# Kernel tuning notes

Hardware: AMD Instinct MI355X
Metric: run time of the kernel (lower is better)

The kernel has to match this reference:

```python
import jax, jax.numpy as jnp
import numpy as np

NUM_HEADS = 8
LN_EPS = 1e-5
COS_EPS = 1e-8


def setup_inputs() -> dict:
    key = jax.random.key(0)
    ks = jax.random.split(key, 16)
    B, S, H, C = 16, 4096, 768, 64
    std = 0.02
    f32 = jnp.float32
    return {
        "hidden_states": jax.random.normal(ks[0], (B, S, H), f32),
        "concept_embeddings": jax.random.normal(ks[1], (C, H), f32),
        "Wq": jax.random.normal(ks[2], (H, H), f32) * std,
        "bq": jnp.zeros((H,), f32),
        "Wk": jax.random.normal(ks[3], (H, H), f32) * std,
        "bk": jnp.zeros((H,), f32),
        "Wv": jax.random.normal(ks[4], (H, H), f32) * std,
        "bv": jnp.zeros((H,), f32),
        "Wo": jax.random.normal(ks[5], (H, H), f32) * std,
        "bo": jnp.zeros((H,), f32),
        "Wg1": jax.random.normal(ks[6], (3 * H, H), f32) * std,
        "bg1": jnp.zeros((H,), f32),
        "Wg2": jax.random.normal(ks[7], (H, 1), f32) * std,
        "bg2": jnp.zeros((1,), f32),
        "ln_g": jnp.ones((H,), f32),
        "ln_b": jnp.zeros((H,), f32),
    }


def reference(hidden_states, concept_embeddings, Wq, bq, Wk, bk, Wv, bv,
              Wo, bo, Wg1, bg1, Wg2, bg2, ln_g, ln_b):
    B, S, H = hidden_states.shape
    C = concept_embeddings.shape[0]
    NH = NUM_HEADS
    HD = H // NH

    # QKV projections; concepts are shared across the batch
    Q = (hidden_states @ Wq + bq).reshape(B, S, NH, HD)      # [B,S,NH,HD]
    K = (concept_embeddings @ Wk + bk).reshape(C, NH, HD)    # [C,NH,HD]
    V = (concept_embeddings @ Wv + bv).reshape(C, NH, HD)

    scores = jnp.einsum('bshd,chd->bhsc', Q, K) / (HD ** 0.5)  # [B,NH,S,C]
    attn = jax.nn.softmax(scores, axis=-1)  # dropout is eval-mode identity
    context = jnp.einsum('bhsc,chd->bshd', attn, V).reshape(B, S, H)
    context = context @ Wo + bo

    # content relevance: cosine sim of mean-pooled text vs mean-pooled concepts
    text_pooled = hidden_states.mean(axis=1)          # [B,H]
    concept_pooled = concept_embeddings.mean(axis=0)  # [H] (same for all batch)
    num = text_pooled @ concept_pooled                # [B]
    den = jnp.maximum(jnp.linalg.norm(text_pooled, axis=-1), COS_EPS) * \
          jnp.maximum(jnp.linalg.norm(concept_pooled), COS_EPS)
    relevance = num / den                             # [B]
    rel_feat = jnp.broadcast_to(relevance[:, None, None], (B, S, H))

    gate_in = jnp.concatenate([hidden_states, context, rel_feat], axis=-1)  # [B,S,3H]
    gate = jax.nn.sigmoid(jax.nn.relu(gate_in @ Wg1 + bg1) @ Wg2 + bg2)     # [B,S,1]

    out = hidden_states + gate * context
    mu = out.mean(axis=-1, keepdims=True)
    var = out.var(axis=-1, keepdims=True)
    out = (out - mu) / jnp.sqrt(var + LN_EPS) * ln_g + ln_b

    attn_avg = attn.mean(axis=1)  # [B,S,C] for XAI
    return out, attn_avg
```

## Files before the change

### kernel.cpp

```cpp
#include <hip/hip_runtime.h>

typedef __attribute__((ext_vector_type(8))) short bf16x8;
typedef __attribute__((ext_vector_type(4))) float f32x4;
typedef unsigned short u16;

#define MFMA(a,b,c) __builtin_amdgcn_mfma_f32_16x16x32_bf16((a),(b),(c),0,0,0)

__device__ __forceinline__ short f2bf(float f){
  union { float f; unsigned u; } v; v.f = f;
  unsigned r = v.u + 0x7FFFu + ((v.u >> 16) & 1u);
  return (short)(r >> 16);
}
__device__ __forceinline__ float bf2f(short s){
  union { unsigned u; float f; } v; v.u = ((unsigned)(unsigned short)s) << 16; return v.f;
}
__device__ __forceinline__ bf16x8 pack8(f32x4 x, f32x4 y){
  bf16x8 r;
  r[0]=f2bf(x[0]); r[1]=f2bf(x[1]); r[2]=f2bf(x[2]); r[3]=f2bf(x[3]);
  r[4]=f2bf(y[0]); r[5]=f2bf(y[1]); r[6]=f2bf(y[2]); r[7]=f2bf(y[3]);
  return r;
}
__device__ __forceinline__ int pch(int c, int row){ return (c & ~7) | ((c & 7) ^ (row & 7)); }

__device__ __forceinline__ void gload16(void* lp, const void* gp){
  __builtin_amdgcn_global_load_lds((const __attribute__((address_space(1))) unsigned*)gp,
                                   (__attribute__((address_space(3))) unsigned*)lp, 16, 0, 0);
}
__device__ __forceinline__ void stWB(short* buf, const short* img, int half, int w, int lane){
  const char* gp = (const char*)img;
  #pragma unroll
  for (int it=0; it<4; ++it){
    int id = it*256 + w*64 + lane; int r = id>>3, c = id&7;
    gload16((char*)buf + it*4096 + w*1024, gp + r*256 + half*128 + c*16);
  }
}
__device__ __forceinline__ void stA128(short* buf, const u16* rowb, int kstep, int w, int lane){
  #pragma unroll
  for (int it=0; it<4; ++it){
    int id = it*256 + w*64 + lane; int r = id>>3, c = id&7;
    gload16((char*)buf + it*4096 + w*1024, rowb + (size_t)r*1536 + (kstep*8 + c)*8);
  }
}
__device__ __forceinline__ void stA256(short* buf, const u16* rowb, int kstep, int w, int lane){
  int tid = w*64 + lane;
  #pragma unroll
  for (int it=0; it<4; ++it){
    int id = it*512 + tid; int r = id>>3, c = id&7;
    gload16((char*)buf + it*8192 + w*1024, rowb + (size_t)r*1536 + (kstep*8 + c)*8);
  }
}
__device__ __forceinline__ void stB256(short* buf, const short* img, int half, int w, int lane){
  int tid = w*64 + lane;
  #pragma unroll
  for (int it=0; it<4; ++it){
    int id = it*512 + tid; int r = id>>3, c = id&7;
    gload16((char*)buf + it*8192 + w*1024,
            img + (size_t)(r>>7)*98304 + (size_t)(r&127)*128 + half*64 + c*8);
  }
}

__global__ void prep_w(const float* __restrict__ Wg1, short* __restrict__ WaI, short* __restrict__ WbI){
  __shared__ short lt[128][136];
  int blk = blockIdx.x;
  int mat = blk / 36, t = blk % 36, kt = t / 6, jt = t % 6;
  const float* src = (mat==0)? Wg1 : (Wg1 + (size_t)768*768);
  short* dst = (mat==0)? WaI : WbI;
  int tid = threadIdx.x;
  #pragma unroll
  for (int it=0; it<16; ++it){
    int kl = it*8 + (tid>>5);
    int jl = (tid&31)*4;
    f32x4 v = *(const f32x4*)&src[(size_t)(kt*128+kl)*768 + jt*128 + jl];
    lt[jl+0][kl]=f2bf(v[0]); lt[jl+1][kl]=f2bf(v[1]);
    lt[jl+2][kl]=f2bf(v[2]); lt[jl+3][kl]=f2bf(v[3]);
  }
  __syncthreads();
  size_t base = (size_t)(jt*6 + kt)*16384;
  #pragma unroll
  for (int cc=0; cc<8; ++cc){
    int ci = cc*256 + tid;
    int jl = ci >> 4, sc = ci & 15;
    int kkb = ((sc ^ (jl & 7)) << 3);
    bf16x8 v = *(const bf16x8*)&lt[jl][kkb];
    *(bf16x8*)&dst[base + (size_t)jl*128 + sc*8] = v;
  }
}

__global__ __launch_bounds__(256) void prep_kv(const float* __restrict__ ce,
                        const float* __restrict__ Wk, const float* __restrict__ bk,
                        const float* __restrict__ Wv, const float* __restrict__ bv,
                        short* __restrict__ Kc, short* __restrict__ VT){
  __shared__ float sh[8][768];
  int jt = blockIdx.x / 8, cg = blockIdx.x % 8;
  int tid = threadIdx.x;
  int j = jt*64 + (tid & 63);
  int cl = tid >> 6;
  for (int i = tid; i < 8*768; i += 256){
    int c2 = i / 768; int h = i - c2*768;
    sh[c2][h] = ce[(size_t)(cg*8+c2)*768 + h];
  }
  __syncthreads();
  float aK0=0.f, aV0=0.f, aK1=0.f, aV1=0.f;
  #pragma unroll 4
  for (int h=0; h<768; ++h){
    float wk = Wk[(size_t)h*768 + j];
    float wv = Wv[(size_t)h*768 + j];
    float x0 = sh[cl*2][h], x1 = sh[cl*2+1][h];
    aK0 += x0*wk; aV0 += x0*wv;
    aK1 += x1*wk; aV1 += x1*wv;
  }
  float bkj = bk[j], bvj = bv[j];
  int c0 = cg*8 + cl*2;
  Kc[(size_t)c0*768 + j]     = f2bf(aK0 + bkj);
  Kc[(size_t)(c0+1)*768 + j] = f2bf(aK1 + bkj);
  VT[(size_t)j*64 + c0]      = f2bf(aV0 + bvj);
  VT[(size_t)j*64 + c0+1]    = f2bf(aV1 + bvj);
}

__global__ void prep_misc(const float* __restrict__ Wg1, const float* __restrict__ ce,
                          const float* __restrict__ bq, const short* __restrict__ Kc,
                          float* __restrict__ wg1c, float* __restrict__ cp,
                          float* __restrict__ sbias){
  __shared__ float red[4][64];
  int b = blockIdx.x, tid = threadIdx.x;
  if (b < 12){
    int j = b*64 + (tid & 63);
    int kq = tid >> 6;
    float s = 0.f;
    for (int r=0; r<192; ++r)
      s += Wg1[(size_t)(1536 + kq*192 + r)*768 + j];
    red[kq][tid&63] = s;
    __syncthreads();
    if (tid < 64) wg1c[b*64+tid] = red[0][tid]+red[1][tid]+red[2][tid]+red[3][tid];
  } else if (b < 15){
    int h = (b-12)*256 + tid;
    float s = 0.f;
    #pragma unroll
    for (int c2=0; c2<64; ++c2) s += ce[(size_t)c2*768 + h];
    cp[h] = s * (1.f/64.f);
  } else {
    int hc = (b-15)*256 + tid;
    int h = hc >> 6, c = hc & 63;
    float s = 0.f;
    #pragma unroll
    for (int j=0; j<96; ++j)
      s += bq[h*96+j] * bf2f(Kc[(size_t)c*768 + h*96 + j]);
    sbias[hc] = s * 0.10206207262f;
  }
}

__global__ __launch_bounds__(256) void prep_eff(const float* __restrict__ Wq,
                        const short* __restrict__ Kc, short* __restrict__ WeffI){
  __shared__ short KA[64][104];
  __shared__ short WB[128][104];
  int h = blockIdx.x / 6, kt = blockIdx.x % 6, tid = threadIdx.x;
  const int lane = tid & 63, w = tid >> 6, l15 = lane & 15, g = lane >> 4;
  #pragma unroll
  for (int it=0; it<3; ++it){
    int i = it*256 + tid;
    int c = i / 12, cb = i % 12;
    *(bf16x8*)&KA[c][cb*8] = *(const bf16x8*)&Kc[(size_t)c*768 + h*96 + cb*8];
  }
  #pragma unroll
  for (int it=0; it<12; ++it){
    int i = it*256 + tid;
    int d = i / 24, q = i % 24;
    f32x4 v = *(const f32x4*)&Wq[(size_t)(kt*128+d)*768 + h*96 + q*4];
    WB[d][q*4+0]=f2bf(v[0]); WB[d][q*4+1]=f2bf(v[1]);
    WB[d][q*4+2]=f2bf(v[2]); WB[d][q*4+3]=f2bf(v[3]);
  }
  __syncthreads();
  f32x4 acc[4][2];
  #pragma unroll
  for (int i=0;i<4;++i){ acc[i][0]=(f32x4){0,0,0,0}; acc[i][1]=(f32x4){0,0,0,0}; }
  #pragma unroll
  for (int ks=0; ks<3; ++ks){
    bf16x8 a[4], b[2];
    #pragma unroll
    for (int mf=0; mf<4; ++mf) a[mf] = *(const bf16x8*)&KA[mf*16+l15][ks*32+g*8];
    #pragma unroll
    for (int nf=0; nf<2; ++nf) b[nf] = *(const bf16x8*)&WB[w*32+nf*16+l15][ks*32+g*8];
    #pragma unroll
    for (int mf=0; mf<4; ++mf)
      #pragma unroll
      for (int nf=0; nf<2; ++nf)
        acc[mf][nf] = MFMA(a[mf], b[nf], acc[mf][nf]);
  }
  size_t base = (size_t)((h>>1)*6 + kt)*16384;
  #pragma unroll
  for (int mf=0; mf<4; ++mf)
    #pragma unroll
    for (int nf=0; nf<2; ++nf)
      #pragma unroll
      for (int r=0; r<4; ++r){
        int c = mf*16 + g*4 + r;
        int d = w*32 + nf*16 + l15;
        int hcl = (h&1)*64 + c;
        WeffI[base + (size_t)hcl*128 + (((d>>3)^(hcl&7))<<3) + (d&7)] = f2bf(acc[mf][nf][r] * 0.10206207262f);
      }
}

__global__ __launch_bounds__(256) void prep_vwo(const float* __restrict__ Wo,
                        const short* __restrict__ VT, short* __restrict__ VWoI){
  __shared__ short WoT[128][104];
  __shared__ short VA[64][104];
  int h = blockIdx.x / 6, dt = blockIdx.x % 6, tid = threadIdx.x;
  const int lane = tid & 63, w = tid >> 6, l15 = lane & 15, g = lane >> 4;
  #pragma unroll
  for (int it=0; it<12; ++it){
    int i = it*256 + tid;
    int j = i / 32, qd = i % 32;
    f32x4 v = *(const f32x4*)&Wo[(size_t)(h*96+j)*768 + dt*128 + qd*4];
    WoT[qd*4+0][j]=f2bf(v[0]); WoT[qd*4+1][j]=f2bf(v[1]);
    WoT[qd*4+2][j]=f2bf(v[2]); WoT[qd*4+3][j]=f2bf(v[3]);
  }
  #pragma unroll
  for (int it=0; it<3; ++it){
    int i = it*256 + tid;
    int j = i / 8, cb = i % 8;
    bf16x8 v = *(const bf16x8*)&VT[(size_t)(h*96+j)*64 + cb*8];
    #pragma unroll
    for (int x=0; x<8; ++x) VA[cb*8+x][j] = v[x];
  }
  __syncthreads();
  f32x4 acc[2][4];
  #pragma unroll
  for (int i=0;i<2;++i)
    #pragma unroll
    for (int j=0;j<4;++j) acc[i][j]=(f32x4){0,0,0,0};
  #pragma unroll
  for (int ks=0; ks<3; ++ks){
    bf16x8 a[2], b[4];
    #pragma unroll
    for (int mf=0; mf<2; ++mf) a[mf] = *(const bf16x8*)&WoT[w*32+mf*16+l15][ks*32+g*8];
    #pragma unroll
    for (int nf=0; nf<4; ++nf) b[nf] = *(const bf16x8*)&VA[nf*16+l15][ks*32+g*8];
    #pragma unroll
    for (int mf=0; mf<2; ++mf)
      #pragma unroll
      for (int nf=0; nf<4; ++nf)
        acc[mf][nf] = MFMA(a[mf], b[nf], acc[mf][nf]);
  }
  size_t base = (size_t)(dt*4 + (h>>1))*16384;
  #pragma unroll
  for (int mf=0; mf<2; ++mf)
    #pragma unroll
    for (int nf=0; nf<4; ++nf)
      #pragma unroll
      for (int r=0; r<4; ++r){
        int d = w*32 + mf*16 + g*4 + r;
        int c = nf*16 + l15;
        int hcl = (h&1)*64 + c;
        VWoI[base + (size_t)d*128 + (((hcl>>3)^(d&7))<<3) + (hcl&7)] = f2bf(acc[mf][nf][r]);
      }
}

__global__ __launch_bounds__(384) void prep_hs(const float* __restrict__ hs,
                                               float* __restrict__ outp, float* __restrict__ tpp){
  __shared__ float csum[4][768];
  int tid = threadIdx.x;
  int c = tid % 96, rg = tid / 96;
  size_t r0 = (size_t)blockIdx.x * 128;
  u16* holes = (u16*)outp;
  float s[8];
  #pragma unroll
  for (int j=0;j<8;++j) s[j]=0.f;
  #pragma unroll 4
  for (int i=0; i<32; ++i){
    size_t row = r0 + rg*32 + i;
    const float* p = hs + row*768 + c*8;
    f32x4 x = __builtin_nontemporal_load((const f32x4*)p);
    f32x4 y = __builtin_nontemporal_load((const f32x4*)(p+4));
    *(bf16x8*)&holes[row*1536 + pch(c,(int)row)*8] = pack8(x,y);
    #pragma unroll
    for (int j=0;j<4;++j){ s[j]+=x[j]; s[4+j]+=y[j]; }
  }
  #pragma unroll
  for (int j=0;j<8;++j) csum[rg][c*8+j] = s[j];
  __syncthreads();
  for (int cc=tid; cc<768; cc+=384)
    tpp[(size_t)blockIdx.x*768 + cc] = csum[0][cc]+csum[1][cc]+csum[2][cc]+csum[3][cc];
}

__global__ void pool23(const float* __restrict__ tpp, const float* __restrict__ cp,
                       float* __restrict__ rel){
  int b = blockIdx.x;
  float a=0.f, n1=0.f, n2=0.f;
  for (int h = threadIdx.x; h < 768; h += 256){
    float s = 0.f;
    #pragma unroll
    for (int k=0; k<32; ++k) s += tpp[((size_t)b*32 + k)*768 + h];
    s *= (1.f/4096.f);
    float c = cp[h];
    a += s*c; n1 += s*s; n2 += c*c;
  }
  #pragma unroll
  for (int m=1; m<64; m<<=1){ a+=__shfl_xor(a,m); n1+=__shfl_xor(n1,m); n2+=__shfl_xor(n2,m); }
  __shared__ float r3[3][4];
  int w = threadIdx.x >> 6;
  if ((threadIdx.x & 63) == 0){ r3[0][w]=a; r3[1][w]=n1; r3[2][w]=n2; }
  __syncthreads();
  if (threadIdx.x == 0){
    float A = r3[0][0]+r3[0][1]+r3[0][2]+r3[0][3];
    float N1= r3[1][0]+r3[1][1]+r3[1][2]+r3[1][3];
    float N2= r3[2][0]+r3[2][1]+r3[2][2]+r3[2][3];
    rel[b] = A / (fmaxf(sqrtf(N1),1e-8f) * fmaxf(sqrtf(N2),1e-8f));
  }
}

__global__ __launch_bounds__(256) void gs(const short* __restrict__ WeffI,
                                          const float* __restrict__ sbias, float* outp){
  __shared__ short A0[8192], A1[8192], B0[8192], B1[8192];
  const int tid = threadIdx.x, lane = tid & 63, w = tid >> 6;
  const int l15 = lane & 15, g = lane >> 4;
  const int bid = blockIdx.x;
  const int nb = (bid >> 3) & 3, mt = (bid/32)*8 + (bid & 7);
  const int wm = w & 1, wn = w >> 1;
  const size_t t0 = (size_t)mt*128;
  u16* holes = (u16*)outp;
  const u16* Arow = holes + t0*1536;
  const short* Wimg = WeffI + (size_t)nb*6*16384;
  f32x4 acc[4][4];
  #pragma unroll
  for (int i=0;i<4;++i)
    #pragma unroll
    for (int j=0;j<4;++j) acc[i][j] = (f32x4){0.f,0.f,0.f,0.f};
  stA128(A0, Arow, 0, w, lane);
  stWB(B0, Wimg, 0, w, lane);
  __syncthreads();
  #pragma unroll
  for (int ks2=0; ks2<12; ++ks2){
    const short* Ac = (ks2&1)? A1 : A0;
    const short* Bc = (ks2&1)? B1 : B0;
    short* An = (ks2&1)? A0 : A1;
    short* Bn = (ks2&1)? B0 : B1;
    if (ks2<11){
      stA128(An, Arow, ks2+1, w, lane);
      stWB(Bn, Wimg + (size_t)(((ks2+1)>>1))*16384, (ks2+1)&1, w, lane);
    }
    #pragma unroll
    for (int ks=0; ks<2; ++ks){
      bf16x8 a[4], b[4];
      #pragma unroll
      for (int mf=0; mf<4; ++mf){ int r = wm*64+mf*16+l15; a[mf] = *(const bf16x8*)&Ac[r*64 + (((ks*4+g)^(r&7))<<3)]; }
      #pragma unroll
      for (int nf=0; nf<4; ++nf){ int r = wn*64+nf*16+l15; b[nf] = *(const bf16x8*)&Bc[r*64 + (((ks*4+g)^(r&7))<<3)]; }
      #pragma unroll
      for (int mf=0; mf<4; ++mf)
        #pragma unroll
        for (int nf=0; nf<4; ++nf)
          acc[mf][nf] = MFMA(a[mf], b[nf], acc[mf][nf]);
    }
    __syncthreads();
  }
  #pragma unroll
  for (int mf=0; mf<4; ++mf)
    #pragma unroll
    for (int r=0; r<4; ++r){
      float v[4];
      #pragma unroll
      for (int nf=0; nf<4; ++nf)
        v[nf] = acc[mf][nf][r] + sbias[nb*128 + wn*64 + nf*16 + l15];
      float m = fmaxf(fmaxf(v[0],v[1]), fmaxf(v[2],v[3]));
      m = fmaxf(m,__shfl_xor(m,1)); m = fmaxf(m,__shfl_xor(m,2));
      m = fmaxf(m,__shfl_xor(m,4)); m = fmaxf(m,__shfl_xor(m,8));
      float e[4]; float s = 0.f;
      #pragma unroll
      for (int nf=0; nf<4; ++nf){ e[nf] = __expf(v[nf]-m); s += e[nf]; }
      s += __shfl_xor(s,1); s += __shfl_xor(s,2); s += __shfl_xor(s,4); s += __shfl_xor(s,8);
      float inv = 1.f/s;
      int grow = wm*64 + mf*16 + g*4 + r;
      #pragma unroll
      for (int nf=0; nf<4; ++nf){
        int col = nb*128 + wn*64 + nf*16 + l15;
        holes[(t0+grow)*1536 + 768 + pch(col>>3, grow)*8 + (col&7)] = (u16)f2bf(e[nf]*inv);
      }
    }
}

__global__ __launch_bounds__(256) void gvwo(const short* __restrict__ VWoI,
                                            const float* __restrict__ bo, float* outp){
  __shared__ short B0[8192], B1[8192];
  const int tid = threadIdx.x, lane = tid & 63, w = tid >> 6;
  const int l15 = lane & 15, g = lane >> 4;
  const size_t t0 = (size_t)blockIdx.x * 64;
  const int arow = w*16 + l15;
  const int drow = w*16 + g*4;
  u16* holes = (u16*)outp;
  bf16x8 af[16];
  #pragma unroll
  for (int kk=0; kk<16; ++kk){
    int kc = kk*4 + g;
    af[kk] = *(const bf16x8*)&holes[(t0+arow)*1536 + 768 + pch(kc, arow)*8];
  }
  stWB(B0, VWoI, 0, w, lane);
  {
    float s0[8], s1[8];
    #pragma unroll
    for (int j=0;j<8;++j){ s0[j]=0.f; s1[j]=0.f; }
    #pragma unroll
    for (int kk=0; kk<16; kk+=2)
      #pragma unroll
      for (int j=0;j<8;++j) s0[j] += bf2f(af[kk][j]);
    #pragma unroll
    for (int kk=1; kk<16; kk+=2)
      #pragma unroll
      for (int j=0;j<8;++j) s1[j] += bf2f(af[kk][j]);
    float* ap = &outp[(size_t)50331648 + (size_t)(t0+arow)*64];
    f32x4 o;
    #pragma unroll
    for (int j=0;j<4;++j) o[j] = s0[j]*0.125f;
    __builtin_nontemporal_store(o, (f32x4*)(ap + g*8));
    #pragma unroll
    for (int j=0;j<4;++j) o[j] = s0[4+j]*0.125f;
    __builtin_nontemporal_store(o, (f32x4*)(ap + g*8 + 4));
    #pragma unroll
    for (int j=0;j<4;++j) o[j] = s1[j]*0.125f;
    __builtin_nontemporal_store(o, (f32x4*)(ap + (4+g)*8));
    #pragma unroll
    for (int j=0;j<4;++j) o[j] = s1[4+j]*0.125f;
    __builtin_nontemporal_store(o, (f32x4*)(ap + (4+g)*8 + 4));
  }
  __syncthreads();
  #pragma unroll 1
  for (int nb=0; nb<6; ++nb){
    f32x4 acc[8];
    #pragma unroll
    for (int i=0;i<8;++i) acc[i]=(f32x4){0.f,0.f,0.f,0.f};
    #pragma unroll
    for (int ks2=0; ks2<8; ++ks2){
      const short* Bc = (ks2&1)? B1 : B0;
      short* Bn = (ks2&1)? B0 : B1;
      if (ks2<7)       stWB(Bn, VWoI + (size_t)(nb*4 + ((ks2+1)>>1))*16384, (ks2+1)&1, w, lane);
      else if (nb<5)   stWB(Bn, VWoI + (size_t)((nb+1)*4)*16384, 0, w, lane);
      #pragma unroll
      for (int ks=0; ks<2; ++ks){
        bf16x8 a = af[ks2*2 + ks];
        #pragma unroll
        for (int nf=0; nf<8; ++nf){
          int br = nf*16 + l15;
          bf16x8 b = *(const bf16x8*)&Bc[br*64 + (((ks*4+g)^(br&7))<<3)];
          acc[nf] = MFMA(a, b, acc[nf]);
        }
      }
      __syncthreads();
    }
    #pragma unroll
    for (int nf=0; nf<8; ++nf)
      #pragma unroll
      for (int r=0; r<4; ++r){
        int row = drow + r;
        int col = nb*128 + nf*16 + l15;
        float v = acc[nf][r] + bo[col];
        holes[(t0+row)*1536 + 768 + pch(col>>3, row)*8 + (col&7)] = (u16)f2bf(v);
      }
  }
}

__global__ void __launch_bounds__(512)
__attribute__((amdgpu_waves_per_eu(2, 2))) gate_mm(const short* __restrict__ WaI,
    const short* __restrict__ WbI, const float* __restrict__ bg1,
    const float* __restrict__ wg1c, const float* __restrict__ Wg2,
    const float* __restrict__ rel, float* __restrict__ gpart, float* outp){
  extern __shared__ char lds[];
  short* A0 = (short*)lds;
  short* A1 = (short*)(lds + 32768);
  short* B0 = (short*)(lds + 65536);
  short* B1 = (short*)(lds + 98304);
  const int tid = threadIdx.x, lane = tid & 63, w = tid >> 6;
  const int l15 = lane & 15, g = lane >> 4;
  const int bid = blockIdx.x;
  const int nb = (bid >> 3) % 3, mt = (bid/24)*8 + (bid & 7);
  const int wm = w & 1, wn = w >> 1;
  const size_t t0 = (size_t)mt*256;
  const float relb = rel[t0 >> 12];
  u16* holes = (u16*)outp;
  const u16* h1p = holes + t0*1536;
  const u16* h2p = h1p + 768;
  f32x4 acc[8][4];
  #pragma unroll
  for (int i=0;i<8;++i)
    #pragma unroll
    for (int j=0;j<4;++j) acc[i][j]=(f32x4){0.f,0.f,0.f,0.f};
  stA256(A0, h1p, 0, w, lane);
  stB256(B0, WaI + (size_t)(nb*2)*98304, 0, w, lane);
  __syncthreads();
  #pragma unroll 1
  for (int pass=0; pass<2; ++pass){
    const short* Wimg = pass ? (WbI + (size_t)(nb*2)*98304) : (WaI + (size_t)(nb*2)*98304);
    const u16* Ap = pass ? h2p : h1p;
    #pragma unroll
    for (int ks2=0; ks2<12; ++ks2){
      const short* Ac = (ks2&1)? A1 : A0;
      const short* Bc = (ks2&1)? B1 : B0;
      short* An = (ks2&1)? A0 : A1;
      short* Bn = (ks2&1)? B0 : B1;
      if (ks2<11){
        stA256(An, Ap, ks2+1, w, lane);
        stB256(Bn, Wimg + (size_t)((ks2+1)>>1)*16384, (ks2+1)&1, w, lane);
      } else if (pass==0){
        stA256(An, h2p, 0, w, lane);
        stB256(Bn, WbI + (size_t)(nb*2)*98304, 0, w, lane);
      }
      #pragma unroll
      for (int ks=0; ks<2; ++ks){
        bf16x8 a[8], b[4];
        #pragma unroll
        for (int mf=0; mf<8; ++mf){ int r = wm*128+mf*16+l15; a[mf] = *(const bf16x8*)&Ac[r*64 + (((ks*4+g)^(r&7))<<3)]; }
        #pragma unroll
        for (int nf=0; nf<4; ++nf){ int r = wn*64+nf*16+l15; b[nf] = *(const bf16x8*)&Bc[r*64 + (((ks*4+g)^(r&7))<<3)]; }
        #pragma unroll
        for (int mf=0; mf<8; ++mf)
          #pragma unroll
          for (int nf=0; nf<4; ++nf)
            acc[mf][nf] = MFMA(a[mf], b[nf], acc[mf][nf]);
      }
      __syncthreads();
    }
  }
  float gp[8][4];
  #pragma unroll
  for (int mf=0; mf<8; ++mf)
    #pragma unroll
    for (int r=0; r<4; ++r) gp[mf][r]=0.f;
  #pragma unroll
  for (int mf=0; mf<8; ++mf)
    #pragma unroll
    for (int nf=0; nf<4; ++nf)
      #pragma unroll
      for (int r=0; r<4; ++r){
        int col = nb*256 + wn*64 + nf*16 + l15;
        gp[mf][r] += fmaxf(acc[mf][nf][r] + bg1[col] + relb*wg1c[col], 0.f) * Wg2[col];
      }
  #pragma unroll
  for (int mf=0; mf<8; ++mf)
    #pragma unroll
    for (int r=0; r<4; ++r){
      float v = gp[mf][r];
      v += __shfl_xor(v,1); v += __shfl_xor(v,2); v += __shfl_xor(v,4); v += __shfl_xor(v,8);
      gp[mf][r] = v;
    }
  float* gred = (float*)lds;
  if (l15 == 0)
    #pragma unroll
    for (int mf=0; mf<8; ++mf)
      #pragma unroll
      for (int r=0; r<4; ++r)
        gred[wn*256 + wm*128 + mf*16 + g*4 + r] = gp[mf][r];
  __syncthreads();
  if (tid < 256)
    gpart[(size_t)nb*65536 + t0 + tid] = gred[tid] + gred[256+tid] + gred[512+tid] + gred[768+tid];
}

__global__ __launch_bounds__(256) void lnk(const float* __restrict__ gpart,
    const float* __restrict__ bg2, const float* __restrict__ lng,
    const float* __restrict__ lnb, float* outp){
  const int tid = threadIdx.x, lane = tid & 63, w = tid >> 6;
  u16* holes = (u16*)outp;
  const float bg2v = bg2[0];
  #pragma unroll 1
  for (int i=0; i<8; ++i){
    int row = blockIdx.x*32 + w*8 + i;
    float gsum = bg2v;
    #pragma unroll
    for (int nb2=0; nb2<3; ++nb2) gsum += gpart[(size_t)nb2*65536 + row];
    float gg = 1.f/(1.f + __expf(-gsum));
    int c1 = lane, c2 = 64 + (lane & 31);
    size_t rb = (size_t)row*1536;
    bf16x8 hv1 = __builtin_nontemporal_load((const bf16x8*)&holes[rb + pch(c1,row)*8]);
    bf16x8 ov1 = __builtin_nontemporal_load((const bf16x8*)&holes[rb + 768 + pch(c1,row)*8]);
    bf16x8 hv2 = __builtin_nontemporal_load((const bf16x8*)&holes[rb + pch(c2,row)*8]);
    bf16x8 ov2 = __builtin_nontemporal_load((const bf16x8*)&holes[rb + 768 + pch(c2,row)*8]);
    float x1[8], x2[8];
    float sum=0.f, sq=0.f;
    #pragma unroll
    for (int j=0;j<8;++j){ float x = bf2f(hv1[j]) + gg*bf2f(ov1[j]); x1[j]=x; sum+=x; sq+=x*x; }
    if (lane < 32){
      #pragma unroll
      for (int j=0;j<8;++j){ float x = bf2f(hv2[j]) + gg*bf2f(ov2[j]); x2[j]=x; sum+=x; sq+=x*x; }
    }
    #pragma unroll
    for (int m=1; m<64; m<<=1){ sum += __shfl_xor(sum,m); sq += __shfl_xor(sq,m); }
    float mu = sum * (1.f/768.f);
    float var = sq * (1.f/768.f) - mu*mu;
    float rs = rsqrtf(var + 1e-5f);
    {
      f32x4 ga = *(const f32x4*)&lng[c1*8], gb = *(const f32x4*)&lng[c1*8+4];
      f32x4 ba = *(const f32x4*)&lnb[c1*8], bb = *(const f32x4*)&lnb[c1*8+4];
      f32x4 o0, o1;
      #pragma unroll
      for (int j=0;j<4;++j){ o0[j] = (x1[j]-mu)*rs*ga[j]+ba[j]; o1[j] = (x1[4+j]-mu)*rs*gb[j]+bb[j]; }
      __builtin_nontemporal_store(o0, (f32x4*)&outp[(size_t)row*768 + c1*8]);
      __builtin_nontemporal_store(o1, (f32x4*)&outp[(size_t)row*768 + c1*8 + 4]);
    }
    if (lane < 32){
      f32x4 ga = *(const f32x4*)&lng[c2*8], gb = *(const f32x4*)&lng[c2*8+4];
      f32x4 ba = *(const f32x4*)&lnb[c2*8], bb = *(const f32x4*)&lnb[c2*8+4];
      f32x4 o0, o1;
      #pragma unroll
      for (int j=0;j<4;++j){ o0[j] = (x2[j]-mu)*rs*ga[j]+ba[j]; o1[j] = (x2[4+j]-mu)*rs*gb[j]+bb[j]; }
      __builtin_nontemporal_store(o0, (f32x4*)&outp[(size_t)row*768 + c2*8]);
      __builtin_nontemporal_store(o1, (f32x4*)&outp[(size_t)row*768 + c2*8 + 4]);
    }
  }
}

extern "C" void kernel_launch(void* const* d_in, const int* in_sizes, int n_in,
                              void* d_out, int out_size, void* d_ws, size_t ws_size,
                              hipStream_t stream) {
  (void)in_sizes; (void)n_in; (void)out_size; (void)ws_size;
  const float* hs  = (const float*)d_in[0];
  const float* ce  = (const float*)d_in[1];
  const float* Wq  = (const float*)d_in[2];
  const float* bq  = (const float*)d_in[3];
  const float* Wk  = (const float*)d_in[4];
  const float* bk  = (const float*)d_in[5];
  const float* Wv  = (const float*)d_in[6];
  const float* bv  = (const float*)d_in[7];
  const float* Wo  = (const float*)d_in[8];
  const float* bo  = (const float*)d_in[9];
  const float* Wg1 = (const float*)d_in[10];
  const float* bg1 = (const float*)d_in[11];
  const float* Wg2 = (const float*)d_in[12];
  const float* bg2 = (const float*)d_in[13];
  const float* lng = (const float*)d_in[14];
  const float* lnb = (const float*)d_in[15];
  char* ws = (char*)d_ws;
  short* WeffI = (short*)(ws + 0);
  short* VWoI  = (short*)(ws + 1179648);
  short* WaI   = (short*)(ws + 2359296);
  short* WbI   = (short*)(ws + 3538944);
  short* Kc    = (short*)(ws + 4718592);
  short* VT    = (short*)(ws + 4816896);
  float* wg1c  = (float*)(ws + 4915200);
  float* cp    = (float*)(ws + 4918272);
  float* rel   = (float*)(ws + 4970496);
  float* tpp   = (float*)(ws + 4970752);
  float* gpart = (float*)(ws + 4970752);
  float* sbias = (float*)(ws + 6543616);
  float* outp  = (float*)d_out;

  prep_kv  <<<96,  256, 0, stream>>>(ce, Wk, bk, Wv, bv, Kc, VT);
  prep_w   <<<72,  256, 0, stream>>>(Wg1, WaI, WbI);
  prep_misc<<<17,  256, 0, stream>>>(Wg1, ce, bq, Kc, wg1c, cp, sbias);
  prep_eff <<<48,  256, 0, stream>>>(Wq, Kc, WeffI);
  prep_vwo <<<48,  256, 0, stream>>>(Wo, VT, VWoI);
  prep_hs  <<<512, 384, 0, stream>>>(hs, outp, tpp);
  pool23   <<<16,  256, 0, stream>>>(tpp, cp, rel);
  gs       <<<2048,256, 0, stream>>>(WeffI, sbias, outp);
  gvwo     <<<1024,256, 0, stream>>>(VWoI, bo, outp);
  hipFuncSetAttribute(reinterpret_cast<const void*>(gate_mm),
                      hipFuncAttributeMaxDynamicSharedMemorySize, 131072);
  gate_mm  <<<768, 512, 131072, stream>>>(WaI, WbI, bg1, wg1c, Wg2, rel, gpart, outp);
  lnk      <<<2048,256, 0, stream>>>(gpart, bg2, lng, lnb, outp);
}
```

Measured before the change: 500.6 us.

## Merge prep kernels into two launches and enlarge score GEMM tiles to 256x256

Five small prep kernels are folded into two multi-role kernels (prep1, prep2) that branch on block index, cutting launch count and dependency gaps. The score GEMM gs is replaced by gs256, which uses 512 threads, 256x256 tiles with 8x4 MFMA accumulators per wave, and 128KB of dynamic LDS. Larger tiles raise operand reuse and cut block count, but add register pressure and lower occupancy. Dependency order is kept because prep2 runs after prep1, which produces Kc and VT.

```diff
diff --git a/kernel.cpp b/kernel.cpp
--- a/kernel.cpp
+++ b/kernel.cpp
@@ -34,13 +34,6 @@
     gload16((char*)buf + it*4096 + w*1024, gp + r*256 + half*128 + c*16);
   }
 }
-__device__ __forceinline__ void stA128(short* buf, const u16* rowb, int kstep, int w, int lane){
-  #pragma unroll
-  for (int it=0; it<4; ++it){
-    int id = it*256 + w*64 + lane; int r = id>>3, c = id&7;
-    gload16((char*)buf + it*4096 + w*1024, rowb + (size_t)r*1536 + (kstep*8 + c)*8);
-  }
-}
 __device__ __forceinline__ void stA256(short* buf, const u16* rowb, int kstep, int w, int lane){
   int tid = w*64 + lane;
   #pragma unroll
@@ -59,200 +52,202 @@
   }
 }
 
-__global__ void prep_w(const float* __restrict__ Wg1, short* __restrict__ WaI, short* __restrict__ WbI){
-  __shared__ short lt[128][136];
-  int blk = blockIdx.x;
-  int mat = blk / 36, t = blk % 36, kt = t / 6, jt = t % 6;
-  const float* src = (mat==0)? Wg1 : (Wg1 + (size_t)768*768);
-  short* dst = (mat==0)? WaI : WbI;
-  int tid = threadIdx.x;
-  #pragma unroll
-  for (int it=0; it<16; ++it){
-    int kl = it*8 + (tid>>5);
-    int jl = (tid&31)*4;
-    f32x4 v = *(const f32x4*)&src[(size_t)(kt*128+kl)*768 + jt*128 + jl];
-    lt[jl+0][kl]=f2bf(v[0]); lt[jl+1][kl]=f2bf(v[1]);
-    lt[jl+2][kl]=f2bf(v[2]); lt[jl+3][kl]=f2bf(v[3]);
-  }
-  __syncthreads();
-  size_t base = (size_t)(jt*6 + kt)*16384;
-  #pragma unroll
-  for (int cc=0; cc<8; ++cc){
-    int ci = cc*256 + tid;
-    int jl = ci >> 4, sc = ci & 15;
-    int kkb = ((sc ^ (jl & 7)) << 3);
-    bf16x8 v = *(const bf16x8*)&lt[jl][kkb];
-    *(bf16x8*)&dst[base + (size_t)jl*128 + sc*8] = v;
-  }
-}
-
-__global__ __launch_bounds__(256) void prep_kv(const float* __restrict__ ce,
-                        const float* __restrict__ Wk, const float* __restrict__ bk,
-                        const float* __restrict__ Wv, const float* __restrict__ bv,
-                        short* __restrict__ Kc, short* __restrict__ VT){
-  __shared__ float sh[8][768];
-  int jt = blockIdx.x / 8, cg = blockIdx.x % 8;
-  int tid = threadIdx.x;
-  int j = jt*64 + (tid & 63);
-  int cl = tid >> 6;
-  for (int i = tid; i < 8*768; i += 256){
-    int c2 = i / 768; int h = i - c2*768;
-    sh[c2][h] = ce[(size_t)(cg*8+c2)*768 + h];
-  }
-  __syncthreads();
-  float aK0=0.f, aV0=0.f, aK1=0.f, aV1=0.f;
-  #pragma unroll 4
-  for (int h=0; h<768; ++h){
-    float wk = Wk[(size_t)h*768 + j];
-    float wv = Wv[(size_t)h*768 + j];
-    float x0 = sh[cl*2][h], x1 = sh[cl*2+1][h];
-    aK0 += x0*wk; aV0 += x0*wv;
-    aK1 += x1*wk; aV1 += x1*wv;
-  }
-  float bkj = bk[j], bvj = bv[j];
-  int c0 = cg*8 + cl*2;
-  Kc[(size_t)c0*768 + j]     = f2bf(aK0 + bkj);
-  Kc[(size_t)(c0+1)*768 + j] = f2bf(aK1 + bkj);
-  VT[(size_t)j*64 + c0]      = f2bf(aV0 + bvj);
-  VT[(size_t)j*64 + c0+1]    = f2bf(aV1 + bvj);
-}
-
-__global__ void prep_misc(const float* __restrict__ Wg1, const float* __restrict__ ce,
-                          const float* __restrict__ bq, const short* __restrict__ Kc,
-                          float* __restrict__ wg1c, float* __restrict__ cp,
-                          float* __restrict__ sbias){
-  __shared__ float red[4][64];
+__global__ __launch_bounds__(256) void prep1(const float* __restrict__ ce,
+    const float* __restrict__ Wk, const float* __restrict__ bk,
+    const float* __restrict__ Wv, const float* __restrict__ bv,
+    const float* __restrict__ Wg1, short* __restrict__ Kc, short* __restrict__ VT,
+    short* __restrict__ WaI, short* __restrict__ WbI){
+  __shared__ float smemf[8704];
   int b = blockIdx.x, tid = threadIdx.x;
-  if (b < 12){
-    int j = b*64 + (tid & 63);
-    int kq = tid >> 6;
-    float s = 0.f;
-    for (int r=0; r<192; ++r)
-      s += Wg1[(size_t)(1536 + kq*192 + r)*768 + j];
-    red[kq][tid&63] = s;
+  if (b < 96){
+    float* sh = smemf;
+    int jt = b / 8, cg = b % 8;
+    int j = jt*64 + (tid & 63);
+    int cl = tid >> 6;
+    for (int i = tid; i < 8*768; i += 256){
+      int c2 = i / 768; int h = i - c2*768;
+      sh[c2*768 + h] = ce[(size_t)(cg*8+c2)*768 + h];
+    }
     __syncthreads();
-    if (tid < 64) wg1c[b*64+tid] = red[0][tid]+red[1][tid]+red[2][tid]+red[3][tid];
-  } else if (b < 15){
-    int h = (b-12)*256 + tid;
-    float s = 0.f;
-    #pragma unroll
-    for (int c2=0; c2<64; ++c2) s += ce[(size_t)c2*768 + h];
-    cp[h] = s * (1.f/64.f);
+    float aK0=0.f, aV0=0.f, aK1=0.f, aV1=0.f;
+    #pragma unroll 4
+    for (int h=0; h<768; ++h){
+      float wk = Wk[(size_t)h*768 + j];
+      float wv = Wv[(size_t)h*768 + j];
+      float x0 = sh[(cl*2)*768 + h], x1 = sh[(cl*2+1)*768 + h];
+      aK0 += x0*wk; aV0 += x0*wv;
+      aK1 += x1*wk; aV1 += x1*wv;
+    }
+    float bkj = bk[j], bvj = bv[j];
+    int c0 = cg*8 + cl*2;
+    Kc[(size_t)c0*768 + j]     = f2bf(aK0 + bkj);
+    Kc[(size_t)(c0+1)*768 + j] = f2bf(aK1 + bkj);
+    VT[(size_t)j*64 + c0]      = f2bf(aV0 + bvj);
+    VT[(size_t)j*64 + c0+1]    = f2bf(aV1 + bvj);
   } else {
-    int hc = (b-15)*256 + tid;
-    int h = hc >> 6, c = hc & 63;
-    float s = 0.f;
-    #pragma unroll
-    for (int j=0; j<96; ++j)
-      s += bq[h*96+j] * bf2f(Kc[(size_t)c*768 + h*96 + j]);
-    sbias[hc] = s * 0.10206207262f;
-  }
-}
-
-__global__ __launch_bounds__(256) void prep_eff(const float* __restrict__ Wq,
-                        const short* __restrict__ Kc, short* __restrict__ WeffI){
-  __shared__ short KA[64][104];
-  __shared__ short WB[128][104];
-  int h = blockIdx.x / 6, kt = blockIdx.x % 6, tid = threadIdx.x;
-  const int lane = tid & 63, w = tid >> 6, l15 = lane & 15, g = lane >> 4;
-  #pragma unroll
-  for (int it=0; it<3; ++it){
-    int i = it*256 + tid;
-    int c = i / 12, cb = i % 12;
-    *(bf16x8*)&KA[c][cb*8] = *(const bf16x8*)&Kc[(size_t)c*768 + h*96 + cb*8];
-  }
-  #pragma unroll
-  for (int it=0; it<12; ++it){
-    int i = it*256 + tid;
-    int d = i / 24, q = i % 24;
-    f32x4 v = *(const f32x4*)&Wq[(size_t)(kt*128+d)*768 + h*96 + q*4];
-    WB[d][q*4+0]=f2bf(v[0]); WB[d][q*4+1]=f2bf(v[1]);
-    WB[d][q*4+2]=f2bf(v[2]); WB[d][q*4+3]=f2bf(v[3]);
-  }
-  __syncthreads();
-  f32x4 acc[4][2];
-  #pragma unroll
-  for (int i=0;i<4;++i){ acc[i][0]=(f32x4){0,0,0,0}; acc[i][1]=(f32x4){0,0,0,0}; }
-  #pragma unroll
-  for (int ks=0; ks<3; ++ks){
-    bf16x8 a[4], b[2];
-    #pragma unroll
-    for (int mf=0; mf<4; ++mf) a[mf] = *(const bf16x8*)&KA[mf*16+l15][ks*32+g*8];
-    #pragma unroll
-    for (int nf=0; nf<2; ++nf) b[nf] = *(const bf16x8*)&WB[w*32+nf*16+l15][ks*32+g*8];
+    short* lt = (short*)smemf;
+    int blk = b - 96;
+    int mat = blk / 36, t = blk % 36, kt = t / 6, jt = t % 6;
+    const float* src = (mat==0)? Wg1 : (Wg1 + (size_t)768*768);
+    short* dst = (mat==0)? WaI : WbI;
+    #pragma unroll
+    for (int it=0; it<16; ++it){
+      int kl = it*8 + (tid>>5);
+      int jl = (tid&31)*4;
+      f32x4 v = *(const f32x4*)&src[(size_t)(kt*128+kl)*768 + jt*128 + jl];
+      lt[(jl+0)*136+kl]=f2bf(v[0]); lt[(jl+1)*136+kl]=f2bf(v[1]);
+      lt[(jl+2)*136+kl]=f2bf(v[2]); lt[(jl+3)*136+kl]=f2bf(v[3]);
+    }
+    __syncthreads();
+    size_t base = (size_t)(jt*6 + kt)*16384;
+    #pragma unroll
+    for (int cc=0; cc<8; ++cc){
+      int ci = cc*256 + tid;
+      int jl = ci >> 4, sc = ci & 15;
+      int kkb = ((sc ^ (jl & 7)) << 3);
+      bf16x8 v = *(const bf16x8*)&lt[jl*136 + kkb];
+      *(bf16x8*)&dst[base + (size_t)jl*128 + sc*8] = v;
+    }
+  }
+}
+
+__global__ __launch_bounds__(256) void prep2(const float* __restrict__ Wg1,
+    const float* __restrict__ ce, const float* __restrict__ bq,
+    const short* __restrict__ Kc, const float* __restrict__ Wq,
+    const float* __restrict__ Wo, const short* __restrict__ VT,
+    float* __restrict__ wg1c, float* __restrict__ cp, float* __restrict__ sbias,
+    short* __restrict__ WeffI, short* __restrict__ VWoI){
+  __shared__ float smemf[9984];
+  int b = blockIdx.x, tid = threadIdx.x;
+  if (b < 17){
+    float* red = smemf;
+    if (b < 12){
+      int j = b*64 + (tid & 63);
+      int kq = tid >> 6;
+      float s = 0.f;
+      for (int r=0; r<192; ++r)
+        s += Wg1[(size_t)(1536 + kq*192 + r)*768 + j];
+      red[kq*64 + (tid&63)] = s;
+      __syncthreads();
+      if (tid < 64) wg1c[b*64+tid] = red[tid]+red[64+tid]+red[128+tid]+red[192+tid];
+    } else if (b < 15){
+      int h = (b-12)*256 + tid;
+      float s = 0.f;
+      #pragma unroll
+      for (int c2=0; c2<64; ++c2) s += ce[(size_t)c2*768 + h];
+      cp[h] = s * (1.f/64.f);
+    } else {
+      int hc = (b-15)*256 + tid;
+      int h = hc >> 6, c = hc & 63;
+      float s = 0.f;
+      #pragma unroll
+      for (int j=0; j<96; ++j)
+        s += bq[h*96+j] * bf2f(Kc[(size_t)c*768 + h*96 + j]);
+      sbias[hc] = s * 0.10206207262f;
+    }
+  } else if (b < 65){
+    short* KA = (short*)smemf;
+    short* WB = KA + 6656;
+    int e = b - 17;
+    int h = e / 6, kt = e % 6;
+    const int lane = tid & 63, w = tid >> 6, l15 = lane & 15, g = lane >> 4;
+    #pragma unroll
+    for (int it=0; it<3; ++it){
+      int i = it*256 + tid;
+      int c = i / 12, cb = i % 12;
+      *(bf16x8*)&KA[c*104 + cb*8] = *(const bf16x8*)&Kc[(size_t)c*768 + h*96 + cb*8];
+    }
+    #pragma unroll
+    for (int it=0; it<12; ++it){
+      int i = it*256 + tid;
+      int d = i / 24, q = i % 24;
+      f32x4 v = *(const f32x4*)&Wq[(size_t)(kt*128+d)*768 + h*96 + q*4];
+      WB[d*104 + q*4+0]=f2bf(v[0]); WB[d*104 + q*4+1]=f2bf(v[1]);
+      WB[d*104 + q*4+2]=f2bf(v[2]); WB[d*104 + q*4+3]=f2bf(v[3]);
+    }
+    __syncthreads();
+    f32x4 acc[4][2];
+    #pragma unroll
+    for (int i=0;i<4;++i){ acc[i][0]=(f32x4){0,0,0,0}; acc[i][1]=(f32x4){0,0,0,0}; }
+    #pragma unroll
+    for (int ks=0; ks<3; ++ks){
+      bf16x8 a[4], bb[2];
+      #pragma unroll
+      for (int mf=0; mf<4; ++mf) a[mf] = *(const bf16x8*)&KA[(mf*16+l15)*104 + ks*32+g*8];
+      #pragma unroll
+      for (int nf=0; nf<2; ++nf) bb[nf] = *(const bf16x8*)&WB[(w*32+nf*16+l15)*104 + ks*32+g*8];
+      #pragma unroll
+      for (int mf=0; mf<4; ++mf)
+        #pragma unroll
+        for (int nf=0; nf<2; ++nf)
+          acc[mf][nf] = MFMA(a[mf], bb[nf], acc[mf][nf]);
+    }
+    size_t base = (size_t)((h>>1)*6 + kt)*16384;
     #pragma unroll
     for (int mf=0; mf<4; ++mf)
       #pragma unroll
       for (int nf=0; nf<2; ++nf)
-        acc[mf][nf] = MFMA(a[mf], b[nf], acc[mf][nf]);
-  }
-  size_t base = (size_t)((h>>1)*6 + kt)*16384;
-  #pragma unroll
-  for (int mf=0; mf<4; ++mf)
-    #pragma unroll
-    for (int nf=0; nf<2; ++nf)
-      #pragma unroll
-      for (int r=0; r<4; ++r){
-        int c = mf*16 + g*4 + r;
-        int d = w*32 + nf*16 + l15;
-        int hcl = (h&1)*64 + c;
-        WeffI[base + (size_t)hcl*128 + (((d>>3)^(hcl&7))<<3) + (d&7)] = f2bf(acc[mf][nf][r] * 0.10206207262f);
-      }
-}
-
-__global__ __launch_bounds__(256) void prep_vwo(const float* __restrict__ Wo,
-                        const short* __restrict__ VT, short* __restrict__ VWoI){
-  __shared__ short WoT[128][104];
-  __shared__ short VA[64][104];
-  int h = blockIdx.x / 6, dt = blockIdx.x % 6, tid = threadIdx.x;
-  const int lane = tid & 63, w = tid >> 6, l15 = lane & 15, g = lane >> 4;
-  #pragma unroll
-  for (int it=0; it<12; ++it){
-    int i = it*256 + tid;
-    int j = i / 32, qd = i % 32;
-    f32x4 v = *(const f32x4*)&Wo[(size_t)(h*96+j)*768 + dt*128 + qd*4];
-    WoT[qd*4+0][j]=f2bf(v[0]); WoT[qd*4+1][j]=f2bf(v[1]);
-    WoT[qd*4+2][j]=f2bf(v[2]); WoT[qd*4+3][j]=f2bf(v[3]);
-  }
-  #pragma unroll
-  for (int it=0; it<3; ++it){
-    int i = it*256 + tid;
-    int j = i / 8, cb = i % 8;
-    bf16x8 v = *(const bf16x8*)&VT[(size_t)(h*96+j)*64 + cb*8];
-    #pragma unroll
-    for (int x=0; x<8; ++x) VA[cb*8+x][j] = v[x];
-  }
-  __syncthreads();
-  f32x4 acc[2][4];
-  #pragma unroll
-  for (int i=0;i<2;++i)
-    #pragma unroll
-    for (int j=0;j<4;++j) acc[i][j]=(f32x4){0,0,0,0};
-  #pragma unroll
-  for (int ks=0; ks<3; ++ks){
-    bf16x8 a[2], b[4];
-    #pragma unroll
-    for (int mf=0; mf<2; ++mf) a[mf] = *(const bf16x8*)&WoT[w*32+mf*16+l15][ks*32+g*8];
-    #pragma unroll
-    for (int nf=0; nf<4; ++nf) b[nf] = *(const bf16x8*)&VA[nf*16+l15][ks*32+g*8];
+        #pragma unroll
+        for (int r=0; r<4; ++r){
+          int c = mf*16 + g*4 + r;
+          int d = w*32 + nf*16 + l15;
+          int hcl = (h&1)*64 + c;
+          WeffI[base + (size_t)hcl*128 + (((d>>3)^(hcl&7))<<3) + (d&7)] = f2bf(acc[mf][nf][r] * 0.10206207262f);
+        }
+  } else {
+    short* WoT = (short*)smemf;
+    short* VA  = WoT + 13312;
+    int e = b - 65;
+    int h = e / 6, dt = e % 6;
+    const int lane = tid & 63, w = tid >> 6, l15 = lane & 15, g = lane >> 4;
+    #pragma unroll
+    for (int it=0; it<12; ++it){
+      int i = it*256 + tid;
+      int j = i / 32, qd = i % 32;
+      f32x4 v = *(const f32x4*)&Wo[(size_t)(h*96+j)*768 + dt*128 + qd*4];
+      WoT[(qd*4+0)*104 + j]=f2bf(v[0]); WoT[(qd*4+1)*104 + j]=f2bf(v[1]);
+      WoT[(qd*4+2)*104 + j]=f2bf(v[2]); WoT[(qd*4+3)*104 + j]=f2bf(v[3]);
+    }
+    #pragma unroll
+    for (int it=0; it<3; ++it){
+      int i = it*256 + tid;
+      int j = i / 8, cb = i % 8;
+      bf16x8 v = *(const bf16x8*)&VT[(size_t)(h*96+j)*64 + cb*8];
+      #pragma unroll
+      for (int x=0; x<8; ++x) VA[(cb*8+x)*104 + j] = v[x];
+    }
+    __syncthreads();
+    f32x4 acc[2][4];
+    #pragma unroll
+    for (int i=0;i<2;++i)
+      #pragma unroll
+      for (int j=0;j<4;++j) acc[i][j]=(f32x4){0,0,0,0};
+    #pragma unroll
+    for (int ks=0; ks<3; ++ks){
+      bf16x8 a[2], bb[4];
+      #pragma unroll
+      for (int mf=0; mf<2; ++mf) a[mf] = *(const bf16x8*)&WoT[(w*32+mf*16+l15)*104 + ks*32+g*8];
+      #pragma unroll
+      for (int nf=0; nf<4; ++nf) bb[nf] = *(const bf16x8*)&VA[(nf*16+l15)*104 + ks*32+g*8];
+      #pragma unroll
+      for (int mf=0; mf<2; ++mf)
+        #pragma unroll
+        for (int nf=0; nf<4; ++nf)
+          acc[mf][nf] = MFMA(a[mf], bb[nf], acc[mf][nf]);
+    }
+    size_t base = (size_t)(dt*4 + (h>>1))*16384;
     #pragma unroll
     for (int mf=0; mf<2; ++mf)
       #pragma unroll
       for (int nf=0; nf<4; ++nf)
-        acc[mf][nf] = MFMA(a[mf], b[nf], acc[mf][nf]);
-  }
-  size_t base = (size_t)(dt*4 + (h>>1))*16384;
-  #pragma unroll
-  for (int mf=0; mf<2; ++mf)
-    #pragma unroll
-    for (int nf=0; nf<4; ++nf)
-      #pragma unroll
-      for (int r=0; r<4; ++r){
-        int d = w*32 + mf*16 + g*4 + r;
-        int c = nf*16 + l15;
-        int hcl = (h&1)*64 + c;
-        VWoI[base + (size_t)d*128 + (((hcl>>3)^(d&7))<<3) + (hcl&7)] = f2bf(acc[mf][nf][r]);
-      }
+        #pragma unroll
+        for (int r=0; r<4; ++r){
+          int d = w*32 + mf*16 + g*4 + r;
+          int c = nf*16 + l15;
+          int hcl = (h&1)*64 + c;
+          VWoI[base + (size_t)d*128 + (((hcl>>3)^(d&7))<<3) + (hcl&7)] = f2bf(acc[mf][nf][r]);
+        }
+  }
 }
 
 __global__ __launch_bounds__(384) void prep_hs(const float* __restrict__ hs,
@@ -308,25 +303,30 @@
   }
 }
 
-__global__ __launch_bounds__(256) void gs(const short* __restrict__ WeffI,
-                                          const float* __restrict__ sbias, float* outp){
-  __shared__ short A0[8192], A1[8192], B0[8192], B1[8192];
+__global__ void __launch_bounds__(512)
+__attribute__((amdgpu_waves_per_eu(2, 2))) gs256(const short* __restrict__ WeffI,
+    const float* __restrict__ sbias, float* outp){
+  extern __shared__ char lds[];
+  short* A0 = (short*)lds;
+  short* A1 = (short*)(lds + 32768);
+  short* B0 = (short*)(lds + 65536);
+  short* B1 = (short*)(lds + 98304);
   const int tid = threadIdx.x, lane = tid & 63, w = tid >> 6;
   const int l15 = lane & 15, g = lane >> 4;
   const int bid = blockIdx.x;
-  const int nb = (bid >> 3) & 3, mt = (bid/32)*8 + (bid & 7);
+  const int nb = (bid >> 3) & 1, mt = (bid >> 4)*8 + (bid & 7);
   const int wm = w & 1, wn = w >> 1;
-  const size_t t0 = (size_t)mt*128;
+  const size_t t0 = (size_t)mt*256;
   u16* holes = (u16*)outp;
-  const u16* Arow = holes + t0*1536;
-  const short* Wimg = WeffI + (size_t)nb*6*16384;
-  f32x4 acc[4][4];
-  #pragma unroll
-  for (int i=0;i<4;++i)
-    #pragma unroll
-    for (int j=0;j<4;++j) acc[i][j] = (f32x4){0.f,0.f,0.f,0.f};
-  stA128(A0, Arow, 0, w, lane);
-  stWB(B0, Wimg, 0, w, lane);
+  const u16* h1p = holes + t0*1536;
+  const short* Wimg = WeffI + (size_t)(nb*2)*98304;
+  f32x4 acc[8][4];
+  #pragma unroll
+  for (int i=0;i<8;++i)
+    #pragma unroll
+    for (int j=0;j<4;++j) acc[i][j]=(f32x4){0.f,0.f,0.f,0.f};
+  stA256(A0, h1p, 0, w, lane);
+  stB256(B0, Wimg, 0, w, lane);
   __syncthreads();
   #pragma unroll
   for (int ks2=0; ks2<12; ++ks2){
@@ -335,18 +335,18 @@
     short* An = (ks2&1)? A0 : A1;
     short* Bn = (ks2&1)? B0 : B1;
     if (ks2<11){
-      stA128(An, Arow, ks2+1, w, lane);
-      stWB(Bn, Wimg + (size_t)(((ks2+1)>>1))*16384, (ks2+1)&1, w, lane);
+      stA256(An, h1p, ks2+1, w, lane);
+      stB256(Bn, Wimg + (size_t)((ks2+1)>>1)*16384, (ks2+1)&1, w, lane);
     }
     #pragma unroll
     for (int ks=0; ks<2; ++ks){
-      bf16x8 a[4], b[4];
-      #pragma unroll
-      for (int mf=0; mf<4; ++mf){ int r = wm*64+mf*16+l15; a[mf] = *(const bf16x8*)&Ac[r*64 + (((ks*4+g)^(r&7))<<3)]; }
+      bf16x8 a[8], b[4];
+      #pragma unroll
+      for (int mf=0; mf<8; ++mf){ int r = wm*128+mf*16+l15; a[mf] = *(const bf16x8*)&Ac[r*64 + (((ks*4+g)^(r&7))<<3)]; }
       #pragma unroll
       for (int nf=0; nf<4; ++nf){ int r = wn*64+nf*16+l15; b[nf] = *(const bf16x8*)&Bc[r*64 + (((ks*4+g)^(r&7))<<3)]; }
       #pragma unroll
-      for (int mf=0; mf<4; ++mf)
+      for (int mf=0; mf<8; ++mf)
         #pragma unroll
         for (int nf=0; nf<4; ++nf)
           acc[mf][nf] = MFMA(a[mf], b[nf], acc[mf][nf]);
@@ -354,13 +354,13 @@
     __syncthreads();
   }
   #pragma unroll
-  for (int mf=0; mf<4; ++mf)
+  for (int mf=0; mf<8; ++mf)
     #pragma unroll
     for (int r=0; r<4; ++r){
       float v[4];
       #pragma unroll
       for (int nf=0; nf<4; ++nf)
-        v[nf] = acc[mf][nf][r] + sbias[nb*128 + wn*64 + nf*16 + l15];
+        v[nf] = acc[mf][nf][r] + sbias[nb*256 + wn*64 + nf*16 + l15];
       float m = fmaxf(fmaxf(v[0],v[1]), fmaxf(v[2],v[3]));
       m = fmaxf(m,__shfl_xor(m,1)); m = fmaxf(m,__shfl_xor(m,2));
       m = fmaxf(m,__shfl_xor(m,4)); m = fmaxf(m,__shfl_xor(m,8));
@@ -369,10 +369,10 @@
       for (int nf=0; nf<4; ++nf){ e[nf] = __expf(v[nf]-m); s += e[nf]; }
       s += __shfl_xor(s,1); s += __shfl_xor(s,2); s += __shfl_xor(s,4); s += __shfl_xor(s,8);
       float inv = 1.f/s;
-      int grow = wm*64 + mf*16 + g*4 + r;
+      int grow = wm*128 + mf*16 + g*4 + r;
       #pragma unroll
       for (int nf=0; nf<4; ++nf){
-        int col = nb*128 + wn*64 + nf*16 + l15;
+        int col = nb*256 + wn*64 + nf*16 + l15;
         holes[(t0+grow)*1536 + 768 + pch(col>>3, grow)*8 + (col&7)] = (u16)f2bf(e[nf]*inv);
       }
     }
@@ -640,17 +640,16 @@
   float* sbias = (float*)(ws + 6543616);
   float* outp  = (float*)d_out;
 
-  prep_kv  <<<96,  256, 0, stream>>>(ce, Wk, bk, Wv, bv, Kc, VT);
-  prep_w   <<<72,  256, 0, stream>>>(Wg1, WaI, WbI);
-  prep_misc<<<17,  256, 0, stream>>>(Wg1, ce, bq, Kc, wg1c, cp, sbias);
-  prep_eff <<<48,  256, 0, stream>>>(Wq, Kc, WeffI);
-  prep_vwo <<<48,  256, 0, stream>>>(Wo, VT, VWoI);
-  prep_hs  <<<512, 384, 0, stream>>>(hs, outp, tpp);
-  pool23   <<<16,  256, 0, stream>>>(tpp, cp, rel);
-  gs       <<<2048,256, 0, stream>>>(WeffI, sbias, outp);
-  gvwo     <<<1024,256, 0, stream>>>(VWoI, bo, outp);
+  prep1   <<<168, 256, 0, stream>>>(ce, Wk, bk, Wv, bv, Wg1, Kc, VT, WaI, WbI);
+  prep2   <<<113, 256, 0, stream>>>(Wg1, ce, bq, Kc, Wq, Wo, VT, wg1c, cp, sbias, WeffI, VWoI);
+  prep_hs <<<512, 384, 0, stream>>>(hs, outp, tpp);
+  pool23  <<<16,  256, 0, stream>>>(tpp, cp, rel);
+  hipFuncSetAttribute(reinterpret_cast<const void*>(gs256),
+                      hipFuncAttributeMaxDynamicSharedMemorySize, 131072);
+  gs256   <<<512, 512, 131072, stream>>>(WeffI, sbias, outp);
+  gvwo    <<<1024,256, 0, stream>>>(VWoI, bo, outp);
   hipFuncSetAttribute(reinterpret_cast<const void*>(gate_mm),
                       hipFuncAttributeMaxDynamicSharedMemorySize, 131072);
-  gate_mm  <<<768, 512, 131072, stream>>>(WaI, WbI, bg1, wg1c, Wg2, rel, gpart, outp);
-  lnk      <<<2048,256, 0, stream>>>(gpart, bg2, lng, lnb, outp);
-}
+  gate_mm <<<768, 512, 131072, stream>>>(WaI, WbI, bg1, wg1c, Wg2, rel, gpart, outp);
+  lnk     <<<2048,256, 0, stream>>>(gpart, bg2, lng, lnb, outp);
+}
```

Measured after the change: 491.1 us. No clear change (-1.9%).
